# Optimization experiments

Hardware: AMD Instinct MI355X
Metric: run time of the kernel (lower is better)

## Reference

```python
import jax, jax.numpy as jnp
import numpy as np

TEMPERATURE = 0.05   # distiller.temperature
KD_WEIGHT = 1.0      # args.kd_weight
EPS = 1e-8
B, D = 128, 768


def _huber(diff):
    a = jnp.abs(diff)
    return jnp.where(a < 1.0, 0.5 * a * a, a - 0.5)


def _pairwise_sqdist(x):
    # ||xi||^2 + ||xj||^2 - 2 xi.xj  (squared euclidean, as in source)
    n2 = (x * x).sum(axis=1, keepdims=True)
    return n2 + n2.T - 2.0 * (x @ x.T)


def _distance_loss(s, t):
    ds = _pairwise_sqdist(s)          # [N,N]
    dt = _pairwise_sqdist(t)
    n = ds.shape[0]
    mask = jnp.triu(jnp.ones((n, n), bool), k=1)
    cnt = n * (n - 1) / 2.0
    mean_sd = jax.lax.stop_gradient(jnp.where(mask, ds, 0.0).sum() / cnt) + EPS
    mean_td = jnp.where(mask, dt, 0.0).sum() / cnt + EPS  # teacher is constant anyway
    loss = _huber(ds / mean_sd - dt / mean_td)
    return jnp.where(mask, loss, 0.0).sum() / cnt


def _angle_potentials(x):
    # diffs[i,j] = x[j] - x[i]; unit vectors; cos[i,j,k] = e[i,j] . e[k,j]
    diffs = x[None, :, :] - x[:, None, :]                       # [N,N,D]
    e = diffs / (jnp.linalg.norm(diffs, axis=-1, keepdims=True) + EPS)
    return jnp.einsum('ijd,kjd->ijk', e, e)                     # [N,N,N]


def _angle_loss(s, t):
    ps = _angle_potentials(s)
    pt = _angle_potentials(t)
    n = ps.shape[0]
    i = jnp.arange(n)
    # valid iff i != j, i != k, j != k  (matches the three masked diagonals)
    m = ((i[:, None, None] != i[None, :, None]) &
         (i[:, None, None] != i[None, None, :]) &
         (i[None, :, None] != i[None, None, :]))
    cnt = n * (n - 1) * (n - 2)
    return jnp.where(m, _huber(ps - pt), 0.0).sum() / cnt


def _contrastive_loss(sq, sp):
    scores = (sq @ sp.T) / TEMPERATURE                          # [B,B]
    tgt = jnp.arange(scores.shape[0])                           # * (B//B) == arange
    logZ = jax.nn.logsumexp(scores, axis=-1)
    return (logZ - jnp.take_along_axis(scores, tgt[:, None], axis=1)[:, 0]).mean()


def setup_inputs() -> dict:
    key = jax.random.key(0)
    k1, k2, k3, k4 = jax.random.split(key, 4)
    return {
        'student_qry': jax.random.normal(k1, (B, D), jnp.float32),
        'student_pos': jax.random.normal(k2, (B, D), jnp.float32),
        'teacher_qry': jax.random.normal(k3, (B, D), jnp.float32),
        'teacher_pos': jax.random.normal(k4, (B, D), jnp.float32),
    }


def reference(student_qry, student_pos, teacher_qry, teacher_pos):
    contrastive = _contrastive_loss(student_qry, student_pos)
    s = jnp.concatenate([student_qry, student_pos], axis=0)     # [2B,D]
    t = jnp.concatenate([teacher_qry, teacher_pos], axis=0)
    t = jax.lax.stop_gradient(t)                                # teacher under no_grad
    kd = 0.5 * _distance_loss(s, t) + 0.5 * _angle_loss(s, t)
    total = contrastive + KD_WEIGHT * kd
    return total, contrastive, kd
```

## Files before the change

kernel.cpp:

```cpp
#include <hip/hip_runtime.h>
#include <math.h>

#define N2   256
#define DIM  768
#define EPSF 1e-8f

#define OFF_PART  0u
#define OFF_PDIAG 1048576u
#define OFF_TSUM  1052672u
#define OFF_SLOT  1052928u
#define SL_ANG  0
#define SL_DIST 512
#define SL_CON  768

typedef __attribute__((ext_vector_type(8))) short short8;
typedef __attribute__((ext_vector_type(4))) float f32x4;

__device__ inline float wave_reduce_sum(float v) {
    #pragma unroll
    for (int o = 32; o > 0; o >>= 1) v += __shfl_down(v, o, 64);
    return v;
}
__device__ inline float wave_reduce_max(float v) {
    #pragma unroll
    for (int o = 32; o > 0; o >>= 1) v = fmaxf(v, __shfl_down(v, o, 64));
    return v;
}
__device__ inline float block_reduce_sum(float v, volatile float* red) {
    float w = wave_reduce_sum(v);
    __syncthreads();
    if ((threadIdx.x & 63) == 0) red[threadIdx.x >> 6] = w;
    __syncthreads();
    return red[0] + red[1] + red[2] + red[3];
}
__device__ inline const float* rowptr(const float* q, const float* p, int r) {
    return (r < 128) ? (q + r * DIM) : (p + (r - 128) * DIM);
}
__device__ inline unsigned f2bf(float x) {
    union { float f; unsigned u; } v; v.f = x;
    return (v.u + 0x7fffu + ((v.u >> 16) & 1u)) >> 16;
}

__global__ __launch_bounds__(256) void gemm_kernel(
        const float* __restrict__ sq, const float* __restrict__ sp,
        const float* __restrict__ tq, const float* __restrict__ tp,
        float* __restrict__ ws) {
    const int b = blockIdx.x, t = threadIdx.x;
    const int c = b & 7, mat = (b >> 3) & 1, tile = b >> 4;
    const int m0 = (tile >> 2) * 64, n0 = (tile & 3) * 64;
    const float* q = mat ? tq : sq;
    const float* p = mat ? tp : sp;

    __shared__ unsigned short Asb[64][104];
    __shared__ unsigned short Bsb[64][104];
    __shared__ float redg[4];

    const int srow = t >> 2, skq = (t & 3) * 4;
    const int kb = c * 96;
    const float* arow = rowptr(q, p, m0 + srow);
    const float* brow = rowptr(q, p, n0 + srow);
    #pragma unroll
    for (int m = 0; m < 6; ++m) {
        const float4 a4 = *(const float4*)&arow[kb + skq + 16 * m];
        const float4 b4 = *(const float4*)&brow[kb + skq + 16 * m];
        uint2 ap, bp;
        ap.x = f2bf(a4.x) | (f2bf(a4.y) << 16);
        ap.y = f2bf(a4.z) | (f2bf(a4.w) << 16);
        bp.x = f2bf(b4.x) | (f2bf(b4.y) << 16);
        bp.y = f2bf(b4.z) | (f2bf(b4.w) << 16);
        *(uint2*)&Asb[srow][skq + 16 * m] = ap;
        *(uint2*)&Bsb[srow][skq + 16 * m] = bp;
    }
    __syncthreads();

    const int wave = t >> 6, lane = t & 63;
    const int wm = (wave >> 1) * 32, wn = (wave & 1) * 32;
    const int fr = lane & 15;
    const int fk = (lane >> 4) * 8;
    f32x4 acc[2][2] = {{{0.f,0.f,0.f,0.f},{0.f,0.f,0.f,0.f}},
                       {{0.f,0.f,0.f,0.f},{0.f,0.f,0.f,0.f}}};
    #pragma unroll
    for (int kc = 0; kc < 96; kc += 32) {
        const short8 a0 = *(const short8*)&Asb[wm + fr][kc + fk];
        const short8 a1 = *(const short8*)&Asb[wm + 16 + fr][kc + fk];
        const short8 b0 = *(const short8*)&Bsb[wn + fr][kc + fk];
        const short8 b1 = *(const short8*)&Bsb[wn + 16 + fr][kc + fk];
        acc[0][0] = __builtin_amdgcn_mfma_f32_16x16x32_bf16(a0, b0, acc[0][0], 0, 0, 0);
        acc[0][1] = __builtin_amdgcn_mfma_f32_16x16x32_bf16(a0, b1, acc[0][1], 0, 0, 0);
        acc[1][0] = __builtin_amdgcn_mfma_f32_16x16x32_bf16(a1, b0, acc[1][0], 0, 0, 0);
        acc[1][1] = __builtin_amdgcn_mfma_f32_16x16x32_bf16(a1, b1, acc[1][1], 0, 0, 0);
    }

    float* P = ws + OFF_PART + (unsigned)(c * 2 + mat) * 65536u;
    const int crow0 = (lane >> 4) * 4;
    const int ccol = lane & 15;
    float ts = 0.f;
    #pragma unroll
    for (int ar = 0; ar < 2; ++ar)
        #pragma unroll
        for (int bc = 0; bc < 2; ++bc)
            #pragma unroll
            for (int reg = 0; reg < 4; ++reg) {
                const int row = m0 + wm + ar * 16 + crow0 + reg;
                const int col = n0 + wn + bc * 16 + ccol;
                const float v = acc[ar][bc][reg];
                P[row * 256 + col] = v;
                ts += v;
            }
    if (m0 == n0 && wm == wn && (lane >> 4) == (ccol >> 2)) {
        float* PD = ws + OFF_PDIAG + (unsigned)(c * 2 + mat) * 256u;
        const int reg = lane & 3;
        #pragma unroll
        for (int ar = 0; ar < 2; ++ar)
            PD[m0 + wm + ar * 16 + ccol] = acc[ar][ar][reg];
    }
    const float tsum = block_reduce_sum(ts, redg);
    if (t == 0) ws[OFF_TSUM + (unsigned)(mat * 128 + c * 16 + tile)] = tsum;
}

__global__ __launch_bounds__(256) void mega_kernel(float* __restrict__ ws) {
    const float* P  = ws + OFF_PART;
    const float* PD = ws + OFF_PDIAG;
    __shared__ float sGJ[16][68], sTJ[16][68], sIJ[16][68], sITJ[16][68];
    __shared__ float sGI[32][68], sTI[32][68];
    __shared__ float dgS[256], dgT[256];
    __shared__ float red1[4], red2[4], redS[1];
    const int b = blockIdx.x, t = threadIdx.x;

    if (b < 512) {
        const int k0 = (b & 3) * 64;
        const int j0 = ((b >> 2) & 15) * 16;
        const int i0 = (b >> 6) * 32;
        const int jj = t & 15, ii = t >> 4;
        const int i1 = i0 + ii, i2 = i1 + 16, j = j0 + jj;

        {
            float as = 0.f, at_ = 0.f;
            #pragma unroll
            for (int c = 0; c < 8; ++c) {
                as  += PD[c * 512 + t];
                at_ += PD[c * 512 + 256 + t];
            }
            dgS[t] = as; dgT[t] = at_;
        }
        const int r = t >> 4, c4 = (t & 15) * 4;
        float4 gjs = {0,0,0,0}, gjt = {0,0,0,0};
        {
            const unsigned base = (unsigned)((j0 + r) * 256 + k0 + c4);
            #pragma unroll
            for (int c = 0; c < 8; ++c) {
                const float4 a = *(const float4*)&P[c * 131072u + base];
                const float4 e = *(const float4*)&P[c * 131072u + 65536u + base];
                gjs.x += a.x; gjs.y += a.y; gjs.z += a.z; gjs.w += a.w;
                gjt.x += e.x; gjt.y += e.y; gjt.z += e.z; gjt.w += e.w;
            }
        }
        #pragma unroll
        for (int s2 = 0; s2 < 2; ++s2) {
            const int slot = t + 256 * s2;
            const int ri = slot >> 4, ci = (slot & 15) * 4;
            const unsigned base = (unsigned)((i0 + ri) * 256 + k0 + ci);
            float4 gs = {0,0,0,0}, gt = {0,0,0,0};
            #pragma unroll
            for (int c = 0; c < 8; ++c) {
                const float4 a = *(const float4*)&P[c * 131072u + base];
                const float4 e = *(const float4*)&P[c * 131072u + 65536u + base];
                gs.x += a.x; gs.y += a.y; gs.z += a.z; gs.w += a.w;
                gt.x += e.x; gt.y += e.y; gt.z += e.z; gt.w += e.w;
            }
            *(float4*)&sGI[ri][ci] = gs;
            *(float4*)&sTI[ri][ci] = gt;
        }
        float g1s = 0.f, g1t = 0.f, g2s = 0.f, g2t = 0.f;
        #pragma unroll
        for (int c = 0; c < 8; ++c) {
            g1s += P[c * 131072u + (unsigned)(i1 * 256 + j)];
            g1t += P[c * 131072u + 65536u + (unsigned)(i1 * 256 + j)];
            g2s += P[c * 131072u + (unsigned)(i2 * 256 + j)];
            g2t += P[c * 131072u + 65536u + (unsigned)(i2 * 256 + j)];
        }
        __syncthreads();

        {
            const float djs = dgS[j0 + r], djt = dgT[j0 + r];
            float4 ivs, ivt;
            const float* dS = &dgS[k0 + c4];
            const float* dT = &dgT[k0 + c4];
            ivs.x = 1.f / (sqrtf(fmaxf(djs + dS[0] - 2.f * gjs.x, 0.f)) + EPSF);
            ivs.y = 1.f / (sqrtf(fmaxf(djs + dS[1] - 2.f * gjs.y, 0.f)) + EPSF);
            ivs.z = 1.f / (sqrtf(fmaxf(djs + dS[2] - 2.f * gjs.z, 0.f)) + EPSF);
            ivs.w = 1.f / (sqrtf(fmaxf(djs + dS[3] - 2.f * gjs.w, 0.f)) + EPSF);
            ivt.x = 1.f / (sqrtf(fmaxf(djt + dT[0] - 2.f * gjt.x, 0.f)) + EPSF);
            ivt.y = 1.f / (sqrtf(fmaxf(djt + dT[1] - 2.f * gjt.y, 0.f)) + EPSF);
            ivt.z = 1.f / (sqrtf(fmaxf(djt + dT[2] - 2.f * gjt.z, 0.f)) + EPSF);
            ivt.w = 1.f / (sqrtf(fmaxf(djt + dT[3] - 2.f * gjt.w, 0.f)) + EPSF);
            *(float4*)&sGJ[r][c4] = gjs;
            *(float4*)&sTJ[r][c4] = gjt;
            *(float4*)&sIJ[r][c4] = ivs;
            *(float4*)&sITJ[r][c4] = ivt;
        }
        const float Gjj = dgS[j], Tjj = dgT[j];
        const float wis1 = 1.f / (sqrtf(fmaxf(dgS[i1] + Gjj - 2.f * g1s, 0.f)) + EPSF);
        const float wit1 = 1.f / (sqrtf(fmaxf(dgT[i1] + Tjj - 2.f * g1t, 0.f)) + EPSF);
        const float wis2 = 1.f / (sqrtf(fmaxf(dgS[i2] + Gjj - 2.f * g2s, 0.f)) + EPSF);
        const float wit2 = 1.f / (sqrtf(fmaxf(dgT[i2] + Tjj - 2.f * g2t, 0.f)) + EPSF);
        const float as1 = (Gjj - g1s) * wis1;
        const float at1 = (Tjj - g1t) * wit1;
        const float as2 = (Gjj - g2s) * wis2;
        const float at2 = (Tjj - g2t) * wit2;
        __syncthreads();

        float sum1 = 0.f, sum2 = 0.f;
        for (int c = 0; c < 64; c += 4) {
            const float4 gJ  = *(const float4*)&sGJ[jj][c];
            const float4 iJ  = *(const float4*)&sIJ[jj][c];
            const float4 tJ  = *(const float4*)&sTJ[jj][c];
            const float4 itJ = *(const float4*)&sITJ[jj][c];
            const float4 a1 = *(const float4*)&sGI[ii][c];
            const float4 b1 = *(const float4*)&sTI[ii][c];
            const float4 a2 = *(const float4*)&sGI[ii + 16][c];
            const float4 b2 = *(const float4*)&sTI[ii + 16][c];
            const float gJr[4]  = {gJ.x, gJ.y, gJ.z, gJ.w};
            const float iJr[4]  = {iJ.x, iJ.y, iJ.z, iJ.w};
            const float tJr[4]  = {tJ.x, tJ.y, tJ.z, tJ.w};
            const float itJr[4] = {itJ.x, itJ.y, itJ.z, itJ.w};
            const float a1r[4] = {a1.x, a1.y, a1.z, a1.w};
            const float b1r[4] = {b1.x, b1.y, b1.z, b1.w};
            const float a2r[4] = {a2.x, a2.y, a2.z, a2.w};
            const float b2r[4] = {b2.x, b2.y, b2.z, b2.w};
            #pragma unroll
            for (int e = 0; e < 4; ++e) {
                const float ps1 = fmaf(wis1, a1r[e] - gJr[e], as1) * iJr[e];
                const float pt1 = fmaf(wit1, b1r[e] - tJr[e], at1) * itJr[e];
                const float d1 = ps1 - pt1;
                const float ad1 = fabsf(d1);
                const float m1 = fminf(ad1, 1.f);
                sum1 = fmaf(m1, fmaf(-0.5f, m1, ad1), sum1);

                const float ps2 = fmaf(wis2, a2r[e] - gJr[e], as2) * iJr[e];
                const float pt2 = fmaf(wit2, b2r[e] - tJr[e], at2) * itJr[e];
                const float d2 = ps2 - pt2;
                const float ad2 = fabsf(d2);
                const float m2 = fminf(ad2, 1.f);
                sum2 = fmaf(m2, fmaf(-0.5f, m2, ad2), sum2);
            }
        }
        const float v = block_reduce_sum(sum1 + sum2, red1);
        if (t == 0) ws[OFF_SLOT + SL_ANG + b] = v;
    } else if (b < 768) {
        const int i = b - 512, j = t;
        float gs = 0.f, gt = 0.f, djs = 0.f, djt = 0.f, dis = 0.f, dit = 0.f;
        #pragma unroll
        for (int c = 0; c < 8; ++c) {
            gs  += P[c * 131072u + (unsigned)(i * 256 + j)];
            gt  += P[c * 131072u + 65536u + (unsigned)(i * 256 + j)];
            djs += PD[c * 512 + j];
            djt += PD[c * 512 + 256 + j];
            dis += PD[c * 512 + i];
            dit += PD[c * 512 + 256 + i];
        }
        const float ds = fmaxf(dis + djs - 2.f * gs, 0.f);
        const float dt = fmaxf(dit + djt - 2.f * gt, 0.f);

        const float tr_s = block_reduce_sum(djs, red1);
        const float tr_t = block_reduce_sum(djt, red1);
        const float tv = ws[OFF_TSUM + t];
        const float sum_gs = block_reduce_sum((t < 128) ? tv : 0.f, red1);
        const float sum_gt = block_reduce_sum((t >= 128) ? tv : 0.f, red1);
        const float rs = 1.f / ((256.f * tr_s - sum_gs) / 32640.f + EPSF);
        const float rt = 1.f / ((256.f * tr_t - sum_gt) / 32640.f + EPSF);

        const float dd = ds * rs - dt * rt;
        const float a = fabsf(dd);
        const float m = fminf(a, 1.f);
        const float hv = block_reduce_sum((j > i) ? m * fmaf(-0.5f, m, a) : 0.f, red1);
        if (t == 0) ws[OFF_SLOT + SL_DIST + i] = hv;
    } else {
        const int rrow = b - 768, j = t;
        float gs = 0.f;
        if (j >= 128) {
            #pragma unroll
            for (int c = 0; c < 8; ++c)
                gs += P[c * 131072u + (unsigned)(rrow * 256 + j)];
        }
        const float s = (j >= 128) ? 20.f * gs : -INFINITY;
        if (j == 128 + rrow) redS[0] = s;
        float mx0 = wave_reduce_max(s);
        __syncthreads();
        if ((t & 63) == 0) red2[t >> 6] = mx0;
        __syncthreads();
        const float mx = fmaxf(fmaxf(red2[0], red2[1]), fmaxf(red2[2], red2[3]));
        const float e = block_reduce_sum((j >= 128) ? expf(s - mx) : 0.f, red1);
        if (t == 0) ws[OFF_SLOT + SL_CON + rrow] = mx + logf(e) - redS[0];
    }
}

__global__ __launch_bounds__(256) void finalize_kernel(const float* __restrict__ ws,
                                                       float* __restrict__ out) {
    __shared__ float red1[4];
    const int t = threadIdx.x;
    const float* S = ws + OFF_SLOT;
    const float a_ = block_reduce_sum(S[SL_ANG + t] + S[SL_ANG + 256 + t], red1);
    const float d_ = block_reduce_sum(S[SL_DIST + t], red1);
    const float c_ = block_reduce_sum((t < 128) ? S[SL_CON + t] : 0.f, red1);
    if (t == 0) {
        const float contrastive = c_ / 128.f;
        const float dist = d_ / 32640.f;
        const float ang = a_ / 16581120.f;
        const float kd = 0.5f * (dist + ang);
        out[0] = contrastive + kd;
        out[1] = contrastive;
        out[2] = kd;
    }
}

extern "C" void kernel_launch(void* const* d_in, const int* in_sizes, int n_in,
                              void* d_out, int out_size, void* d_ws, size_t ws_size,
                              hipStream_t stream) {
    (void)in_sizes; (void)n_in; (void)out_size; (void)ws_size;
    const float* sq = (const float*)d_in[0];
    const float* sp = (const float*)d_in[1];
    const float* tq = (const float*)d_in[2];
    const float* tp = (const float*)d_in[3];
    float* ws  = (float*)d_ws;
    float* out = (float*)d_out;

    gemm_kernel<<<256, 256, 0, stream>>>(sq, sp, tq, tp, ws);
    mega_kernel<<<896, 256, 0, stream>>>(ws);
    finalize_kernel<<<1, 256, 0, stream>>>(ws, out);
}
```

Measured before the change: 80.54 us.

## Replace split-K Gram partials with full-K per-block tiles and prefetch

```diff
diff --git a/kernel.cpp b/kernel.cpp
--- a/kernel.cpp
+++ b/kernel.cpp
@@ -5,10 +5,10 @@
 #define DIM  768
 #define EPSF 1e-8f
 
-#define OFF_PART  0u
-#define OFF_PDIAG 1048576u
-#define OFF_TSUM  1052672u
-#define OFF_SLOT  1052928u
+#define OFF_G     0u
+#define OFF_DIAG  131072u
+#define OFF_TSUM  131584u
+#define OFF_SLOT  131712u
 #define SL_ANG  0
 #define SL_DIST 512
 #define SL_CON  768
@@ -34,7 +34,7 @@
     return red[0] + red[1] + red[2] + red[3];
 }
 __device__ inline const float* rowptr(const float* q, const float* p, int r) {
-    return (r < 128) ? (q + r * DIM) : (p + (r - 128) * DIM);
+    return (r < 128) ? (r * DIM + q) : ((r - 128) * DIM + p);
 }
 __device__ inline unsigned f2bf(float x) {
     union { float f; unsigned u; } v; v.f = x;
@@ -46,81 +46,82 @@
         const float* __restrict__ tq, const float* __restrict__ tp,
         float* __restrict__ ws) {
     const int b = blockIdx.x, t = threadIdx.x;
-    const int c = b & 7, mat = (b >> 3) & 1, tile = b >> 4;
-    const int m0 = (tile >> 2) * 64, n0 = (tile & 3) * 64;
+    const int mat = b & 1, tile = b >> 1;
+    const int m0 = (tile >> 3) * 32, n0 = (tile & 7) * 32;
     const float* q = mat ? tq : sq;
     const float* p = mat ? tp : sp;
 
-    __shared__ unsigned short Asb[64][104];
-    __shared__ unsigned short Bsb[64][104];
+    __shared__ unsigned short Asb[32][104];
+    __shared__ unsigned short Bsb[32][104];
     __shared__ float redg[4];
 
-    const int srow = t >> 2, skq = (t & 3) * 4;
-    const int kb = c * 96;
-    const float* arow = rowptr(q, p, m0 + srow);
-    const float* brow = rowptr(q, p, n0 + srow);
-    #pragma unroll
-    for (int m = 0; m < 6; ++m) {
-        const float4 a4 = *(const float4*)&arow[kb + skq + 16 * m];
-        const float4 b4 = *(const float4*)&brow[kb + skq + 16 * m];
-        uint2 ap, bp;
-        ap.x = f2bf(a4.x) | (f2bf(a4.y) << 16);
-        ap.y = f2bf(a4.z) | (f2bf(a4.w) << 16);
-        bp.x = f2bf(b4.x) | (f2bf(b4.y) << 16);
-        bp.y = f2bf(b4.z) | (f2bf(b4.w) << 16);
-        *(uint2*)&Asb[srow][skq + 16 * m] = ap;
-        *(uint2*)&Bsb[srow][skq + 16 * m] = bp;
-    }
-    __syncthreads();
+    const int srow = t >> 3, skq = (t & 7) * 12;
+    const float* arow = rowptr(q, p, m0 + srow) + skq;
+    const float* brow = rowptr(q, p, n0 + srow) + skq;
+
+    float4 pa[3], pb[3];
+    #pragma unroll
+    for (int m = 0; m < 3; ++m) {
+        pa[m] = *(const float4*)&arow[4 * m];
+        pb[m] = *(const float4*)&brow[4 * m];
+    }
 
     const int wave = t >> 6, lane = t & 63;
-    const int wm = (wave >> 1) * 32, wn = (wave & 1) * 32;
+    const int wm = (wave >> 1) * 16, wn = (wave & 1) * 16;
     const int fr = lane & 15;
     const int fk = (lane >> 4) * 8;
-    f32x4 acc[2][2] = {{{0.f,0.f,0.f,0.f},{0.f,0.f,0.f,0.f}},
-                       {{0.f,0.f,0.f,0.f},{0.f,0.f,0.f,0.f}}};
-    #pragma unroll
-    for (int kc = 0; kc < 96; kc += 32) {
-        const short8 a0 = *(const short8*)&Asb[wm + fr][kc + fk];
-        const short8 a1 = *(const short8*)&Asb[wm + 16 + fr][kc + fk];
-        const short8 b0 = *(const short8*)&Bsb[wn + fr][kc + fk];
-        const short8 b1 = *(const short8*)&Bsb[wn + 16 + fr][kc + fk];
-        acc[0][0] = __builtin_amdgcn_mfma_f32_16x16x32_bf16(a0, b0, acc[0][0], 0, 0, 0);
-        acc[0][1] = __builtin_amdgcn_mfma_f32_16x16x32_bf16(a0, b1, acc[0][1], 0, 0, 0);
-        acc[1][0] = __builtin_amdgcn_mfma_f32_16x16x32_bf16(a1, b0, acc[1][0], 0, 0, 0);
-        acc[1][1] = __builtin_amdgcn_mfma_f32_16x16x32_bf16(a1, b1, acc[1][1], 0, 0, 0);
-    }
-
-    float* P = ws + OFF_PART + (unsigned)(c * 2 + mat) * 65536u;
+    f32x4 acc = {0.f, 0.f, 0.f, 0.f};
+
+    for (int c = 0; c < 8; ++c) {
+        #pragma unroll
+        for (int m = 0; m < 3; ++m) {
+            uint2 ap, bp;
+            ap.x = f2bf(pa[m].x) | (f2bf(pa[m].y) << 16);
+            ap.y = f2bf(pa[m].z) | (f2bf(pa[m].w) << 16);
+            bp.x = f2bf(pb[m].x) | (f2bf(pb[m].y) << 16);
+            bp.y = f2bf(pb[m].z) | (f2bf(pb[m].w) << 16);
+            *(uint2*)&Asb[srow][skq + 4 * m] = ap;
+            *(uint2*)&Bsb[srow][skq + 4 * m] = bp;
+        }
+        __syncthreads();
+        if (c < 7) {
+            const int kb = (c + 1) * 96;
+            #pragma unroll
+            for (int m = 0; m < 3; ++m) {
+                pa[m] = *(const float4*)&arow[kb + 4 * m];
+                pb[m] = *(const float4*)&brow[kb + 4 * m];
+            }
+        }
+        #pragma unroll
+        for (int kc = 0; kc < 96; kc += 32) {
+            const short8 a0 = *(const short8*)&Asb[wm + fr][kc + fk];
+            const short8 b0 = *(const short8*)&Bsb[wn + fr][kc + fk];
+            acc = __builtin_amdgcn_mfma_f32_16x16x32_bf16(a0, b0, acc, 0, 0, 0);
+        }
+        __syncthreads();
+    }
+
+    float* G = ws + OFF_G + (unsigned)mat * 65536u;
     const int crow0 = (lane >> 4) * 4;
     const int ccol = lane & 15;
     float ts = 0.f;
     #pragma unroll
-    for (int ar = 0; ar < 2; ++ar)
-        #pragma unroll
-        for (int bc = 0; bc < 2; ++bc)
-            #pragma unroll
-            for (int reg = 0; reg < 4; ++reg) {
-                const int row = m0 + wm + ar * 16 + crow0 + reg;
-                const int col = n0 + wn + bc * 16 + ccol;
-                const float v = acc[ar][bc][reg];
-                P[row * 256 + col] = v;
-                ts += v;
-            }
+    for (int reg = 0; reg < 4; ++reg) {
+        const int row = m0 + wm + crow0 + reg;
+        const int col = n0 + wn + ccol;
+        G[row * 256 + col] = acc[reg];
+        ts += acc[reg];
+    }
     if (m0 == n0 && wm == wn && (lane >> 4) == (ccol >> 2)) {
-        float* PD = ws + OFF_PDIAG + (unsigned)(c * 2 + mat) * 256u;
-        const int reg = lane & 3;
-        #pragma unroll
-        for (int ar = 0; ar < 2; ++ar)
-            PD[m0 + wm + ar * 16 + ccol] = acc[ar][ar][reg];
+        ws[OFF_DIAG + (unsigned)(mat * 256 + m0 + wm + ccol)] = acc[ccol & 3];
     }
     const float tsum = block_reduce_sum(ts, redg);
-    if (t == 0) ws[OFF_TSUM + (unsigned)(mat * 128 + c * 16 + tile)] = tsum;
+    if (t == 0) ws[OFF_TSUM + (unsigned)(mat * 64 + tile)] = tsum;
 }
 
 __global__ __launch_bounds__(256) void mega_kernel(float* __restrict__ ws) {
-    const float* P  = ws + OFF_PART;
-    const float* PD = ws + OFF_PDIAG;
+    const float* Pg = ws + OFF_G;
+    const float* Dg = ws + OFF_DIAG;
     __shared__ float sGJ[16][68], sTJ[16][68], sIJ[16][68], sITJ[16][68];
     __shared__ float sGI[32][68], sTI[32][68];
     __shared__ float dgS[256], dgT[256];
@@ -134,51 +135,26 @@
         const int jj = t & 15, ii = t >> 4;
         const int i1 = i0 + ii, i2 = i1 + 16, j = j0 + jj;
 
-        {
-            float as = 0.f, at_ = 0.f;
-            #pragma unroll
-            for (int c = 0; c < 8; ++c) {
-                as  += PD[c * 512 + t];
-                at_ += PD[c * 512 + 256 + t];
-            }
-            dgS[t] = as; dgT[t] = at_;
-        }
+        dgS[t] = Dg[t];
+        dgT[t] = Dg[256 + t];
+
         const int r = t >> 4, c4 = (t & 15) * 4;
-        float4 gjs = {0,0,0,0}, gjt = {0,0,0,0};
-        {
-            const unsigned base = (unsigned)((j0 + r) * 256 + k0 + c4);
-            #pragma unroll
-            for (int c = 0; c < 8; ++c) {
-                const float4 a = *(const float4*)&P[c * 131072u + base];
-                const float4 e = *(const float4*)&P[c * 131072u + 65536u + base];
-                gjs.x += a.x; gjs.y += a.y; gjs.z += a.z; gjs.w += a.w;
-                gjt.x += e.x; gjt.y += e.y; gjt.z += e.z; gjt.w += e.w;
-            }
-        }
+        const unsigned baseJ = (unsigned)((j0 + r) * 256 + k0 + c4);
+        const float4 gjs = *(const float4*)&Pg[baseJ];
+        const float4 gjt = *(const float4*)&Pg[65536u + baseJ];
+
         #pragma unroll
         for (int s2 = 0; s2 < 2; ++s2) {
             const int slot = t + 256 * s2;
             const int ri = slot >> 4, ci = (slot & 15) * 4;
             const unsigned base = (unsigned)((i0 + ri) * 256 + k0 + ci);
-            float4 gs = {0,0,0,0}, gt = {0,0,0,0};
-            #pragma unroll
-            for (int c = 0; c < 8; ++c) {
-                const float4 a = *(const float4*)&P[c * 131072u + base];
-                const float4 e = *(const float4*)&P[c * 131072u + 65536u + base];
-                gs.x += a.x; gs.y += a.y; gs.z += a.z; gs.w += a.w;
-                gt.x += e.x; gt.y += e.y; gt.z += e.z; gt.w += e.w;
-            }
-            *(float4*)&sGI[ri][ci] = gs;
-            *(float4*)&sTI[ri][ci] = gt;
-        }
-        float g1s = 0.f, g1t = 0.f, g2s = 0.f, g2t = 0.f;
-        #pragma unroll
-        for (int c = 0; c < 8; ++c) {
-            g1s += P[c * 131072u + (unsigned)(i1 * 256 + j)];
-            g1t += P[c * 131072u + 65536u + (unsigned)(i1 * 256 + j)];
-            g2s += P[c * 131072u + (unsigned)(i2 * 256 + j)];
-            g2t += P[c * 131072u + 65536u + (unsigned)(i2 * 256 + j)];
-        }
+            *(float4*)&sGI[ri][ci] = *(const float4*)&Pg[base];
+            *(float4*)&sTI[ri][ci] = *(const float4*)&Pg[65536u + base];
+        }
+        const float g1s = Pg[(unsigned)(i1 * 256 + j)];
+        const float g1t = Pg[65536u + (unsigned)(i1 * 256 + j)];
+        const float g2s = Pg[(unsigned)(i2 * 256 + j)];
+        const float g2t = Pg[65536u + (unsigned)(i2 * 256 + j)];
         __syncthreads();
 
         {
@@ -249,24 +225,18 @@
         if (t == 0) ws[OFF_SLOT + SL_ANG + b] = v;
     } else if (b < 768) {
         const int i = b - 512, j = t;
-        float gs = 0.f, gt = 0.f, djs = 0.f, djt = 0.f, dis = 0.f, dit = 0.f;
-        #pragma unroll
-        for (int c = 0; c < 8; ++c) {
-            gs  += P[c * 131072u + (unsigned)(i * 256 + j)];
-            gt  += P[c * 131072u + 65536u + (unsigned)(i * 256 + j)];
-            djs += PD[c * 512 + j];
-            djt += PD[c * 512 + 256 + j];
-            dis += PD[c * 512 + i];
-            dit += PD[c * 512 + 256 + i];
-        }
+        const float gs  = Pg[(unsigned)(i * 256 + j)];
+        const float gt  = Pg[65536u + (unsigned)(i * 256 + j)];
+        const float djs = Dg[j], djt = Dg[256 + j];
+        const float dis = Dg[i], dit = Dg[256 + i];
         const float ds = fmaxf(dis + djs - 2.f * gs, 0.f);
         const float dt = fmaxf(dit + djt - 2.f * gt, 0.f);
 
         const float tr_s = block_reduce_sum(djs, red1);
         const float tr_t = block_reduce_sum(djt, red1);
-        const float tv = ws[OFF_TSUM + t];
-        const float sum_gs = block_reduce_sum((t < 128) ? tv : 0.f, red1);
-        const float sum_gt = block_reduce_sum((t >= 128) ? tv : 0.f, red1);
+        const float tv = (t < 128) ? ws[OFF_TSUM + t] : 0.f;
+        const float sum_gs = block_reduce_sum((t < 64) ? tv : 0.f, red1);
+        const float sum_gt = block_reduce_sum((t >= 64) ? tv : 0.f, red1);
         const float rs = 1.f / ((256.f * tr_s - sum_gs) / 32640.f + EPSF);
         const float rt = 1.f / ((256.f * tr_t - sum_gt) / 32640.f + EPSF);
 
@@ -277,12 +247,7 @@
         if (t == 0) ws[OFF_SLOT + SL_DIST + i] = hv;
     } else {
         const int rrow = b - 768, j = t;
-        float gs = 0.f;
-        if (j >= 128) {
-            #pragma unroll
-            for (int c = 0; c < 8; ++c)
-                gs += P[c * 131072u + (unsigned)(rrow * 256 + j)];
-        }
+        const float gs = (j >= 128) ? Pg[(unsigned)(rrow * 256 + j)] : 0.f;
         const float s = (j >= 128) ? 20.f * gs : -INFINITY;
         if (j == 128 + rrow) redS[0] = s;
         float mx0 = wave_reduce_max(s);
@@ -325,7 +290,7 @@
     float* ws  = (float*)d_ws;
     float* out = (float*)d_out;
 
-    gemm_kernel<<<256, 256, 0, stream>>>(sq, sp, tq, tp, ws);
+    gemm_kernel<<<128, 256, 0, stream>>>(sq, sp, tq, tp, ws);
     mega_kernel<<<896, 256, 0, stream>>>(ws);
     finalize_kernel<<<1, 256, 0, stream>>>(ws, out);
 }
```

Result: faster. 77.70 us (-3.5%).
